# Optimization experiments

Hardware: AMD Instinct MI355X
Metric: run time of the kernel (lower is better)

## Reference

```python
import jax, jax.numpy as jnp
import numpy as np

VOCAB = 128
NUM_PATHS = 100     # num_paths sampled from the lattice
NBEST_SCALE = 0.5   # scale on scores before sampling (k2.random_paths)
TEMPERATURE = 1.0   # logprob temperature before normalization
BLANK = 0           # CTC blank token


def setup_inputs() -> dict:
    key = jax.random.key(0)
    k1, k2, k3, k4 = jax.random.split(key, 4)
    B, T, L = 8, 500, 100
    logits = jax.random.normal(k1, (B, T, VOCAB), jnp.float32)
    emissions = jax.nn.log_softmax(logits, -1)  # acoustic-model log-probs (N, T, C)
    emissions_lengths = jax.random.randint(k2, (B,), 400, T + 1).astype(jnp.int32)
    labels = jax.random.randint(k3, (B, L), 1, VOCAB).astype(jnp.int32)
    labels_length = jax.random.randint(k4, (B,), 80, L + 1).astype(jnp.int32)
    return {"emissions": emissions, "emissions_lengths": emissions_lengths,
            "labels": labels, "labels_length": labels_length}


def _mwer(emissions, emissions_lengths, labels, labels_length):
    B, T, V = emissions.shape
    L = labels.shape[1]
    P = NUM_PATHS
    key = jax.random.key(1)
    # --- N-best path sampling: Gumbel perturbation of nbest_scale-scaled log-probs ---
    u = jax.random.uniform(key, (B, P, T, V), emissions.dtype, 1e-6, 1.0 - 1e-6)
    g = -jnp.log(-jnp.log(u))
    tokens = jnp.argmax(emissions[:, None] * NBEST_SCALE + g, axis=-1)  # (B, P, T)
    frame_mask = jnp.arange(T)[None, None, :] < emissions_lengths[:, None, None]
    # path log-prob under the model (unscaled scores), temperature-scaled
    lp = jnp.take_along_axis(emissions[:, None], tokens[..., None], axis=-1)[..., 0]
    path_logp = jnp.sum(jnp.where(frame_mask, lp, 0.0), axis=-1) / TEMPERATURE  # (B, P)
    # --- CTC collapse (ctc_topo semantics: drop blanks + repeats) into padded hyps ---
    prev = jnp.concatenate([jnp.full_like(tokens[..., :1], -1), tokens[..., :-1]], -1)
    keep = (tokens != BLANK) & (tokens != prev) & frame_mask
    pos = jnp.where(keep, jnp.cumsum(keep, -1) - 1, T)  # dropped frames -> dump slot T
    BP = B * P
    tok2, pos2 = tokens.reshape(BP, T), pos.reshape(BP, T)
    hyp = jnp.full((BP, T + 1), -1, tokens.dtype).at[jnp.arange(BP)[:, None], pos2].set(tok2)[:, :T]
    hyp_len = keep.reshape(BP, T).sum(-1)
    # --- Levenshtein alignment: exact edit distance hyp vs ref (vectorized DP) ---
    refs = jnp.repeat(labels, P, axis=0)             # (BP, L)  hyp_to_ref_map
    ref_len = jnp.repeat(labels_length, P, axis=0)   # (BP,)
    dp0 = jnp.broadcast_to(jnp.arange(L + 1, dtype=jnp.int32), (BP, L + 1))
    js = jnp.arange(L + 1, dtype=jnp.int32)[None, :]

    def step(dp, x):
        h, valid = x  # hyp token (BP,), valid flag (BP,)
        cost = (refs != h[:, None]).astype(jnp.int32)                       # (BP, L)
        cand = jnp.concatenate([dp[:, :1] + 1,
                                jnp.minimum(dp[:, 1:] + 1, dp[:, :-1] + cost)], 1)
        # insertion chain new[j] = min(cand[j], new[j-1]+1) via min-plus prefix
        new = jax.lax.cummin(cand - js, axis=1) + js
        return jnp.where(valid[:, None], new, dp), None

    valid = jnp.arange(T)[:, None] < hyp_len[None, :]  # (T, BP)
    dp, _ = jax.lax.scan(step, dp0, (hyp.T, valid))
    wers = jnp.take_along_axis(dp, ref_len[:, None], 1)[:, 0].reshape(B, P)
    wers = jax.lax.stop_gradient(wers.astype(emissions.dtype))
    # --- MWER: normalize path posteriors per utterance, expected WER, 'mean' ---
    prob = jax.nn.softmax(path_logp, axis=1)
    return jnp.mean(prob * wers)


def reference(emissions, emissions_lengths, labels, labels_length):
    return _mwer(emissions, emissions_lengths, labels, labels_length)
```

## Files before the change

kernel.cpp:

```cpp
#include <hip/hip_runtime.h>
#include <stdint.h>

#define NB 8
#define NP 100
#define NT 500
#define NV 128
#define NBP 800
#define TS 512
#define ES 500
#define PAIRS (NB * NT * 25)

typedef unsigned long long u64;

#define ROTL(x, r) __builtin_amdgcn_alignbit((x), (x), 32 - (r))

__device__ __forceinline__ uint32_t threefry01_lo(uint32_t x0, uint32_t x1) {
  const uint32_t k0 = 0u, k1 = 1u;
  const uint32_t k2 = 0x1BD11BDAu ^ k0 ^ k1;
  x0 += k0; x1 += k1;
#define TF_R(r) { x0 += x1; x1 = ROTL(x1, r); x1 ^= x0; }
  TF_R(13) TF_R(15) TF_R(26) TF_R(6)
  x0 += k1; x1 += k2 + 1u;
  TF_R(17) TF_R(29) TF_R(16) TF_R(24)
  x0 += k2; x1 += k0 + 2u;
  TF_R(13) TF_R(15) TF_R(26) TF_R(6)
  x0 += k0; x1 += k1 + 3u;
  TF_R(17) TF_R(29) TF_R(16) TF_R(24)
  x0 += k1; x1 += k2 + 4u;
  TF_R(13) TF_R(15) TF_R(26) TF_R(6)
  x1 += k0 + 5u;
#undef TF_R
  return x1;
}

__global__ __launch_bounds__(256) void k_sample(
    const float* __restrict__ em, const int* __restrict__ elen,
    uint8_t* __restrict__ tok2, float* __restrict__ lp2t) {
  __shared__ float snw[4][NV + 1];
  const int tid = threadIdx.x;
  const int pi0 = blockIdx.x * 64;
  const int R0 = pi0 / 25;
  for (int i = tid; i < 4 * NV; i += 256) {
    const int r = i >> 7, v = i & 127;
    int R = R0 + r; R = R < NB * NT ? R : NB * NT - 1;
    snw[r][v] = -__builtin_amdgcn_exp2f(em[(size_t)R * NV + v] * -0.7213475204444817f);
  }
  __syncthreads();
  const int gg = blockIdx.x * 256 + tid;
  const int pitem = gg >> 2, q = gg & 3;
  if (pitem >= PAIRS) return;
  const int R = pitem / 25;
  const int pp = pitem - R * 25;
  const int b = R / NT;
  const int t = R - b * NT;
  if (t >= elen[b]) return;
  const int r = R - R0;
  const int vh = q << 5;
  const int bp0 = b * NP + 4 * pp;
  const uint32_t baseA = ((uint32_t)(bp0 * NT + t) << 7) + (uint32_t)vh;
  const uint32_t baseB = baseA + (uint32_t)(NT << 7);
  const uint32_t baseC = baseB + (uint32_t)(NT << 7);
  const uint32_t baseD = baseC + (uint32_t)(NT << 7);
  const float span = (float)(1.0 - 1e-6) - 1e-6f;
  float bvA = 3.0e38f, bvB = 3.0e38f, bvC = 3.0e38f, bvD = 3.0e38f;
  int biA = 0, biB = 0, biC = 0, biD = 0;
#pragma unroll 8
  for (int i = 0; i < 32; i++) {
    const uint32_t rA = threefry01_lo(0u, baseA + (uint32_t)i);
    const uint32_t rB = threefry01_lo(0u, baseB + (uint32_t)i);
    const uint32_t rC = threefry01_lo(0u, baseC + (uint32_t)i);
    const uint32_t rD = threefry01_lo(0u, baseD + (uint32_t)i);
    const float w = snw[r][vh + i];
    const float fA = __uint_as_float((rA >> 9) | 0x3f800000u) - 1.0f;
    const float fB = __uint_as_float((rB >> 9) | 0x3f800000u) - 1.0f;
    const float fC = __uint_as_float((rC >> 9) | 0x3f800000u) - 1.0f;
    const float fD = __uint_as_float((rD >> 9) | 0x3f800000u) - 1.0f;
    const float uA = fmaf(fA, span, 1e-6f);
    const float uB = fmaf(fB, span, 1e-6f);
    const float uC = fmaf(fC, span, 1e-6f);
    const float uD = fmaf(fD, span, 1e-6f);
    const float sA = __log2f(uA) * w;
    const float sB = __log2f(uB) * w;
    const float sC = __log2f(uC) * w;
    const float sD = __log2f(uD) * w;
    if (sA < bvA) { bvA = sA; biA = vh + i; }
    if (sB < bvB) { bvB = sB; biB = vh + i; }
    if (sC < bvC) { bvC = sC; biC = vh + i; }
    if (sD < bvD) { bvD = sD; biD = vh + i; }
  }
#pragma unroll
  for (int off = 1; off <= 2; off <<= 1) {
    float ov; int oi;
    ov = __shfl_xor(bvA, off); oi = __shfl_xor(biA, off);
    if (ov < bvA || (ov == bvA && oi < biA)) { bvA = ov; biA = oi; }
    ov = __shfl_xor(bvB, off); oi = __shfl_xor(biB, off);
    if (ov < bvB || (ov == bvB && oi < biB)) { bvB = ov; biB = oi; }
    ov = __shfl_xor(bvC, off); oi = __shfl_xor(biC, off);
    if (ov < bvC || (ov == bvC && oi < biC)) { bvC = ov; biC = oi; }
    ov = __shfl_xor(bvD, off); oi = __shfl_xor(biD, off);
    if (ov < bvD || (ov == bvD && oi < biD)) { bvD = ov; biD = oi; }
  }
  if (q == 0) {
    const float* __restrict__ erow = em + (size_t)R * NV;
    const float eA = erow[biA], eB = erow[biB], eC = erow[biC], eD = erow[biD];
    tok2[(size_t)(bp0 + 0) * TS + t] = (uint8_t)biA;
    tok2[(size_t)(bp0 + 1) * TS + t] = (uint8_t)biB;
    tok2[(size_t)(bp0 + 2) * TS + t] = (uint8_t)biC;
    tok2[(size_t)(bp0 + 3) * TS + t] = (uint8_t)biD;
    *(float4*)&lp2t[(size_t)t * NBP + bp0] = make_float4(eA, eB, eC, eD);
  }
}

__global__ __launch_bounds__(128) void k_pq(
    const int* __restrict__ labels, const int* __restrict__ llen,
    uint4* __restrict__ pqg) {
  const int b = blockIdx.x;
  const int c = threadIdx.x;
  const int m = llen[b];
  const int* __restrict__ lab = labels + b * 100;
  uint32_t a0 = 0, a1 = 0, a2 = 0, a3 = 0;
  const int e0 = m < 32 ? m : 32, e1 = m < 64 ? m : 64;
  const int e2 = m < 96 ? m : 96, e3 = m;
  for (int i = 0; i < e0; i++)  a0 |= (uint32_t)(lab[i] == c) << i;
  for (int i = 32; i < e1; i++) a1 |= (uint32_t)(lab[i] == c) << (i - 32);
  for (int i = 64; i < e2; i++) a2 |= (uint32_t)(lab[i] == c) << (i - 64);
  for (int i = 96; i < e3; i++) a3 |= (uint32_t)(lab[i] == c) << (i - 96);
  pqg[b * NV + c] = make_uint4(a0, a1, a2, a3);
}

__global__ __launch_bounds__(64) void k_ce(
    const uint8_t* __restrict__ tok2, const uint4* __restrict__ pqg,
    const int* __restrict__ elen, uint4* __restrict__ eqc,
    int* __restrict__ nkept) {
  __shared__ uint4 pqs[NV];
  const int bp = blockIdx.x;
  const int b = bp / NP;
  const int lane = threadIdx.x;
  pqs[lane] = pqg[b * NV + lane];
  pqs[lane + 64] = pqg[b * NV + lane + 64];
  __syncthreads();
  const int el = elen[b];
  const uint8_t* __restrict__ row = tok2 + (size_t)bp * TS;
  uint4* __restrict__ orow = eqc + (size_t)bp * ES;
  int off = 0;
  for (int t0 = 0; t0 < el; t0 += 64) {
    const int t = t0 + lane;
    const bool inb = (t < el);
    const int c = inb ? row[t] : 0;
    const int cp = (t == 0) ? 255 : (inb ? row[t - 1] : 255);
    const bool kept = inb && (c != 0) && (c != cp);
    const u64 mask = __ballot(kept);
    const int idx = off + (int)__builtin_amdgcn_mbcnt_hi(
        (uint32_t)(mask >> 32),
        __builtin_amdgcn_mbcnt_lo((uint32_t)mask, 0u));
    if (kept) orow[idx] = pqs[c];
    off += (int)__popcll(mask);
  }
  if (lane == 0) nkept[bp] = off;
}

__device__ __forceinline__ void loadg(uint4 (&B)[4], int g, const uint4* __restrict__ rowp) {
#pragma unroll
  for (int i = 0; i < 4; i++) {
    int t = g * 4 + i;
    t = t < ES ? t : ES - 1;
    B[i] = rowp[t];
  }
}

__device__ __forceinline__ void procg(const uint4 (&B)[4], int fbase, int nk,
                                      u64 hmask,
                                      u64& Pv0, u64& Pv1, u64& Mv0, u64& Mv1,
                                      int& score, int& scoreFin) {
#pragma unroll
  for (int i = 0; i < 4; i++) {
    const u64 Eq0 = (u64)B[i].x | ((u64)B[i].y << 32);
    const u64 Eq1 = (u64)B[i].z | ((u64)B[i].w << 32);
    const u64 Xv0 = Eq0 | Mv0, Xv1 = Eq1 | Mv1;
    const u64 EP0 = Eq0 & Pv0, EP1 = Eq1 & Pv1;
    const u64 sA = EP0 + Pv0;
    const u64 sB = EP1 + Pv1 + (sA < EP0 ? 1ull : 0ull);
    const u64 Xh0 = (sA ^ Pv0) | Eq0;
    const u64 Xh1 = (sB ^ Pv1) | Eq1;
    const u64 Ph0 = Mv0 | ~(Xh0 | Pv0);
    const u64 Ph1 = Mv1 | ~(Xh1 | Pv1);
    const u64 Mh0 = Pv0 & Xh0, Mh1 = Pv1 & Xh1;
    score += (int)((Ph1 & hmask) != 0) - (int)((Mh1 & hmask) != 0);
    scoreFin = (fbase + i < nk) ? score : scoreFin;
    const u64 nPh1 = (Ph1 << 1) | (Ph0 >> 63);
    const u64 nPh0 = (Ph0 << 1) | 1ull;
    const u64 nMh1 = (Mh1 << 1) | (Mh0 >> 63);
    const u64 nMh0 = (Mh0 << 1);
    Pv0 = nMh0 | ~(Xv0 | nPh0);
    Pv1 = nMh1 | ~(Xv1 | nPh1);
    Mv0 = nPh0 & Xv0;
    Mv1 = nPh1 & Xv1;
  }
}

__global__ __launch_bounds__(64) void k_dp(
    const uint4* __restrict__ eqc, const int* __restrict__ nkept,
    const int* __restrict__ llen, float* __restrict__ wer) {
  const int b = blockIdx.x, h = blockIdx.y;
  const int tid = threadIdx.x;
  const bool active = (tid < 50);
  const int bp = b * NP + h * 50 + (active ? tid : 49);
  const int m = llen[b];
  const int nk = nkept[bp];
  const uint4* __restrict__ rowp = eqc + (size_t)bp * ES;
  u64 Pv0 = ~0ull, Pv1 = ~0ull, Mv0 = 0ull, Mv1 = 0ull;
  int score = m, scoreFin = m;
  const u64 hmask = 1ull << ((m - 1) & 63);

  const int ngl = (nk + 3) >> 2;
  int ngmax = ngl;
  for (int off = 1; off < 64; off <<= 1) {
    const int o = __shfl_xor(ngmax, off);
    ngmax = o > ngmax ? o : ngmax;
  }
  uint4 B0[4], B1[4], B2[4], B3[4];
  loadg(B0, 0, rowp); loadg(B1, 1, rowp);
  loadg(B2, 2, rowp); loadg(B3, 3, rowp);
  int g = 0;
  while (g + 4 <= ngmax) {
    procg(B0, (g    ) * 4, nk, hmask, Pv0, Pv1, Mv0, Mv1, score, scoreFin);
    loadg(B0, g + 4, rowp);
    procg(B1, (g + 1) * 4, nk, hmask, Pv0, Pv1, Mv0, Mv1, score, scoreFin);
    loadg(B1, g + 5, rowp);
    procg(B2, (g + 2) * 4, nk, hmask, Pv0, Pv1, Mv0, Mv1, score, scoreFin);
    loadg(B2, g + 6, rowp);
    procg(B3, (g + 3) * 4, nk, hmask, Pv0, Pv1, Mv0, Mv1, score, scoreFin);
    loadg(B3, g + 7, rowp);
    g += 4;
  }
  if (g     < ngmax) procg(B0, (g    ) * 4, nk, hmask, Pv0, Pv1, Mv0, Mv1, score, scoreFin);
  if (g + 1 < ngmax) procg(B1, (g + 1) * 4, nk, hmask, Pv0, Pv1, Mv0, Mv1, score, scoreFin);
  if (g + 2 < ngmax) procg(B2, (g + 2) * 4, nk, hmask, Pv0, Pv1, Mv0, Mv1, score, scoreFin);
  if (active) wer[bp] = (float)scoreFin;
}

__global__ __launch_bounds__(128) void k_red(
    const float* __restrict__ lp2t, const int* __restrict__ elen,
    double* __restrict__ pred) {
  const int b = blockIdx.x, k = blockIdx.y;
  const int tid = threadIdx.x;
  const bool active = (tid < NP);
  const int p = active ? tid : NP - 1;
  const int el = elen[b];
  const int t0 = k * 125;
  const int t1 = (t0 + 125 < el) ? t0 + 125 : el;
  const float* __restrict__ col = lp2t + b * NP + p;
  double s = 0.0;
#pragma unroll 8
  for (int t = t0; t < t1; t++) s += (double)col[(size_t)t * NBP];
  if (active) pred[(size_t)(b * NP + p) * 4 + k] = s;
}

__global__ __launch_bounds__(512) void k_fin(
    const double* __restrict__ pred, const float* __restrict__ wer,
    float* __restrict__ out) {
  __shared__ float partial[NB];
  const int w = threadIdx.x >> 6, lane = threadIdx.x & 63;
  const int base = w * NP;
  float l0 = -1e30f, l1 = -1e30f;
  if (lane < NP) {
    const double* pr = pred + (size_t)(base + lane) * 4;
    l0 = (float)(pr[0] + pr[1] + pr[2] + pr[3]);
  }
  if (lane + 64 < NP) {
    const double* pr = pred + (size_t)(base + lane + 64) * 4;
    l1 = (float)(pr[0] + pr[1] + pr[2] + pr[3]);
  }
  float mx = fmaxf(l0, l1);
  for (int off = 1; off < 64; off <<= 1) mx = fmaxf(mx, __shfl_xor(mx, off));
  const float e0 = (lane < NP) ? __expf(l0 - mx) : 0.0f;
  const float e1 = (lane + 64 < NP) ? __expf(l1 - mx) : 0.0f;
  const float w0 = (lane < NP) ? wer[base + lane] : 0.0f;
  const float w1 = (lane + 64 < NP) ? wer[base + lane + 64] : 0.0f;
  float s = e0 + e1;
  float a = e0 * w0 + e1 * w1;
  for (int off = 1; off < 64; off <<= 1) {
    s += __shfl_xor(s, off);
    a += __shfl_xor(a, off);
  }
  if (lane == 0) partial[w] = a / s;
  __syncthreads();
  if (threadIdx.x == 0) {
    float tot = 0.0f;
    for (int i = 0; i < NB; i++) tot += partial[i];
    out[0] = tot * (1.0f / (float)NBP);
  }
}

extern "C" void kernel_launch(void* const* d_in, const int* in_sizes, int n_in,
                              void* d_out, int out_size, void* d_ws, size_t ws_size,
                              hipStream_t stream) {
  const float* em     = (const float*)d_in[0];
  const int*   elen   = (const int*)d_in[1];
  const int*   labels = (const int*)d_in[2];
  const int*   llen   = (const int*)d_in[3];
  float* out = (float*)d_out;
  char* ws = (char*)d_ws;
  uint4*   eqc   = (uint4*)ws;
  uint8_t* tok2  = (uint8_t*)(ws + 6400000);
  float*   lp2t  = (float*)(ws + 6809600);
  float*   wer   = (float*)(ws + 8409600);
  double*  pred  = (double*)(ws + 8412800);
  int*     nkept = (int*)(ws + 8438400);
  uint4*   pqg   = (uint4*)(ws + 8441600);

  k_sample<<<dim3((PAIRS * 4 + 255) / 256), dim3(256), 0, stream>>>(em, elen, tok2, lp2t);
  k_pq<<<dim3(NB), dim3(128), 0, stream>>>(labels, llen, pqg);
  k_ce<<<dim3(NBP), dim3(64), 0, stream>>>(tok2, pqg, elen, eqc, nkept);
  k_dp<<<dim3(NB, 2), dim3(64), 0, stream>>>(eqc, nkept, llen, wer);
  k_red<<<dim3(NB, 4), dim3(128), 0, stream>>>(lp2t, elen, pred);
  k_fin<<<dim3(1), dim3(512), 0, stream>>>(pred, wer, out);
}
```

Measured before the change: 228.0 us.

## Merge label-mask and path-logprob reductions into neighboring kernels, pad shared weights

The per-batch label bitmask construction now runs as extra blocks appended to the sampling launch, and the path log-prob column reduction runs as extra blocks alongside the bit-parallel edit-distance kernel. This removes two kernel launches and lets the independent small jobs overlap with larger ones. Shared weights are stored with a padded index to avoid LDS bank conflicts between the four quarter-vocab lanes. The DP step now breaks early past the kept length instead of tracking a masked final score, which adds a data-dependent branch inside the unrolled loop.

```diff
diff --git a/kernel.cpp b/kernel.cpp
--- a/kernel.cpp
+++ b/kernel.cpp
@@ -9,10 +9,13 @@
 #define TS 512
 #define ES 500
 #define PAIRS (NB * NT * 25)
+#define NSB 1563
 
 typedef unsigned long long u64;
 
 #define ROTL(x, r) __builtin_amdgcn_alignbit((x), (x), 32 - (r))
+
+#define SIDX(v) ((v) + ((v) >> 5))
 
 __device__ __forceinline__ uint32_t threefry01_lo(uint32_t x0, uint32_t x1) {
   const uint32_t k0 = 0u, k1 = 1u;
@@ -35,15 +38,34 @@
 
 __global__ __launch_bounds__(256) void k_sample(
     const float* __restrict__ em, const int* __restrict__ elen,
-    uint8_t* __restrict__ tok2, float* __restrict__ lp2t) {
-  __shared__ float snw[4][NV + 1];
+    uint8_t* __restrict__ tok2, float* __restrict__ lp2t,
+    const int* __restrict__ labels, const int* __restrict__ llen,
+    uint4* __restrict__ pqg) {
   const int tid = threadIdx.x;
+  if (blockIdx.x >= NSB) {
+    const int b = blockIdx.x - NSB;
+    if (tid < NV) {
+      const int c = tid;
+      const int m = llen[b];
+      const int* __restrict__ lab = labels + b * 100;
+      uint32_t a0 = 0, a1 = 0, a2 = 0, a3 = 0;
+      const int e0 = m < 32 ? m : 32, e1 = m < 64 ? m : 64;
+      const int e2 = m < 96 ? m : 96, e3 = m;
+      for (int i = 0; i < e0; i++)  a0 |= (uint32_t)(lab[i] == c) << i;
+      for (int i = 32; i < e1; i++) a1 |= (uint32_t)(lab[i] == c) << (i - 32);
+      for (int i = 64; i < e2; i++) a2 |= (uint32_t)(lab[i] == c) << (i - 64);
+      for (int i = 96; i < e3; i++) a3 |= (uint32_t)(lab[i] == c) << (i - 96);
+      pqg[b * NV + c] = make_uint4(a0, a1, a2, a3);
+    }
+    return;
+  }
+  __shared__ float snw[4][NV + 4];
   const int pi0 = blockIdx.x * 64;
   const int R0 = pi0 / 25;
   for (int i = tid; i < 4 * NV; i += 256) {
     const int r = i >> 7, v = i & 127;
     int R = R0 + r; R = R < NB * NT ? R : NB * NT - 1;
-    snw[r][v] = -__builtin_amdgcn_exp2f(em[(size_t)R * NV + v] * -0.7213475204444817f);
+    snw[r][SIDX(v)] = -__builtin_amdgcn_exp2f(em[(size_t)R * NV + v] * -0.7213475204444817f);
   }
   __syncthreads();
   const int gg = blockIdx.x * 256 + tid;
@@ -56,6 +78,7 @@
   if (t >= elen[b]) return;
   const int r = R - R0;
   const int vh = q << 5;
+  const int sbase = vh + q;
   const int bp0 = b * NP + 4 * pp;
   const uint32_t baseA = ((uint32_t)(bp0 * NT + t) << 7) + (uint32_t)vh;
   const uint32_t baseB = baseA + (uint32_t)(NT << 7);
@@ -70,7 +93,7 @@
     const uint32_t rB = threefry01_lo(0u, baseB + (uint32_t)i);
     const uint32_t rC = threefry01_lo(0u, baseC + (uint32_t)i);
     const uint32_t rD = threefry01_lo(0u, baseD + (uint32_t)i);
-    const float w = snw[r][vh + i];
+    const float w = snw[r][sbase + i];
     const float fA = __uint_as_float((rA >> 9) | 0x3f800000u) - 1.0f;
     const float fB = __uint_as_float((rB >> 9) | 0x3f800000u) - 1.0f;
     const float fC = __uint_as_float((rC >> 9) | 0x3f800000u) - 1.0f;
@@ -109,23 +132,6 @@
     tok2[(size_t)(bp0 + 3) * TS + t] = (uint8_t)biD;
     *(float4*)&lp2t[(size_t)t * NBP + bp0] = make_float4(eA, eB, eC, eD);
   }
-}
-
-__global__ __launch_bounds__(128) void k_pq(
-    const int* __restrict__ labels, const int* __restrict__ llen,
-    uint4* __restrict__ pqg) {
-  const int b = blockIdx.x;
-  const int c = threadIdx.x;
-  const int m = llen[b];
-  const int* __restrict__ lab = labels + b * 100;
-  uint32_t a0 = 0, a1 = 0, a2 = 0, a3 = 0;
-  const int e0 = m < 32 ? m : 32, e1 = m < 64 ? m : 64;
-  const int e2 = m < 96 ? m : 96, e3 = m;
-  for (int i = 0; i < e0; i++)  a0 |= (uint32_t)(lab[i] == c) << i;
-  for (int i = 32; i < e1; i++) a1 |= (uint32_t)(lab[i] == c) << (i - 32);
-  for (int i = 64; i < e2; i++) a2 |= (uint32_t)(lab[i] == c) << (i - 64);
-  for (int i = 96; i < e3; i++) a3 |= (uint32_t)(lab[i] == c) << (i - 96);
-  pqg[b * NV + c] = make_uint4(a0, a1, a2, a3);
 }
 
 __global__ __launch_bounds__(64) void k_ce(
@@ -171,9 +177,10 @@
 __device__ __forceinline__ void procg(const uint4 (&B)[4], int fbase, int nk,
                                       u64 hmask,
                                       u64& Pv0, u64& Pv1, u64& Mv0, u64& Mv1,
-                                      int& score, int& scoreFin) {
+                                      int& score) {
 #pragma unroll
   for (int i = 0; i < 4; i++) {
+    if (fbase + i >= nk) break;
     const u64 Eq0 = (u64)B[i].x | ((u64)B[i].y << 32);
     const u64 Eq1 = (u64)B[i].z | ((u64)B[i].w << 32);
     const u64 Xv0 = Eq0 | Mv0, Xv1 = Eq1 | Mv1;
@@ -186,7 +193,6 @@
     const u64 Ph1 = Mv1 | ~(Xh1 | Pv1);
     const u64 Mh0 = Pv0 & Xh0, Mh1 = Pv1 & Xh1;
     score += (int)((Ph1 & hmask) != 0) - (int)((Mh1 & hmask) != 0);
-    scoreFin = (fbase + i < nk) ? score : scoreFin;
     const u64 nPh1 = (Ph1 << 1) | (Ph0 >> 63);
     const u64 nPh0 = (Ph0 << 1) | 1ull;
     const u64 nMh1 = (Mh1 << 1) | (Mh0 >> 63);
@@ -198,18 +204,37 @@
   }
 }
 
-__global__ __launch_bounds__(64) void k_dp(
+__global__ __launch_bounds__(128) void k_dpred(
     const uint4* __restrict__ eqc, const int* __restrict__ nkept,
-    const int* __restrict__ llen, float* __restrict__ wer) {
-  const int b = blockIdx.x, h = blockIdx.y;
+    const int* __restrict__ llen, const float* __restrict__ lp2t,
+    const int* __restrict__ elen, float* __restrict__ wer,
+    double* __restrict__ pred) {
+  const int blk = blockIdx.x;
   const int tid = threadIdx.x;
+  if (blk >= 16) {
+    const int i = blk - 16;
+    const int b = i >> 2, k = i & 3;
+    const bool active = (tid < NP);
+    const int p = active ? tid : NP - 1;
+    const int el = elen[b];
+    const int t0 = k * 125;
+    const int t1 = (t0 + 125 < el) ? t0 + 125 : el;
+    const float* __restrict__ col = lp2t + b * NP + p;
+    double s = 0.0;
+#pragma unroll 8
+    for (int t = t0; t < t1; t++) s += (double)col[(size_t)t * NBP];
+    if (active) pred[(size_t)(b * NP + p) * 4 + k] = s;
+    return;
+  }
+  if (tid >= 64) return;
+  const int b = blk >> 1, h = blk & 1;
   const bool active = (tid < 50);
   const int bp = b * NP + h * 50 + (active ? tid : 49);
   const int m = llen[b];
   const int nk = nkept[bp];
   const uint4* __restrict__ rowp = eqc + (size_t)bp * ES;
   u64 Pv0 = ~0ull, Pv1 = ~0ull, Mv0 = 0ull, Mv1 = 0ull;
-  int score = m, scoreFin = m;
+  int score = m;
   const u64 hmask = 1ull << ((m - 1) & 63);
 
   const int ngl = (nk + 3) >> 2;
@@ -223,37 +248,20 @@
   loadg(B2, 2, rowp); loadg(B3, 3, rowp);
   int g = 0;
   while (g + 4 <= ngmax) {
-    procg(B0, (g    ) * 4, nk, hmask, Pv0, Pv1, Mv0, Mv1, score, scoreFin);
+    procg(B0, (g    ) * 4, nk, hmask, Pv0, Pv1, Mv0, Mv1, score);
     loadg(B0, g + 4, rowp);
-    procg(B1, (g + 1) * 4, nk, hmask, Pv0, Pv1, Mv0, Mv1, score, scoreFin);
+    procg(B1, (g + 1) * 4, nk, hmask, Pv0, Pv1, Mv0, Mv1, score);
     loadg(B1, g + 5, rowp);
-    procg(B2, (g + 2) * 4, nk, hmask, Pv0, Pv1, Mv0, Mv1, score, scoreFin);
+    procg(B2, (g + 2) * 4, nk, hmask, Pv0, Pv1, Mv0, Mv1, score);
     loadg(B2, g + 6, rowp);
-    procg(B3, (g + 3) * 4, nk, hmask, Pv0, Pv1, Mv0, Mv1, score, scoreFin);
+    procg(B3, (g + 3) * 4, nk, hmask, Pv0, Pv1, Mv0, Mv1, score);
     loadg(B3, g + 7, rowp);
     g += 4;
   }
-  if (g     < ngmax) procg(B0, (g    ) * 4, nk, hmask, Pv0, Pv1, Mv0, Mv1, score, scoreFin);
-  if (g + 1 < ngmax) procg(B1, (g + 1) * 4, nk, hmask, Pv0, Pv1, Mv0, Mv1, score, scoreFin);
-  if (g + 2 < ngmax) procg(B2, (g + 2) * 4, nk, hmask, Pv0, Pv1, Mv0, Mv1, score, scoreFin);
-  if (active) wer[bp] = (float)scoreFin;
-}
-
-__global__ __launch_bounds__(128) void k_red(
-    const float* __restrict__ lp2t, const int* __restrict__ elen,
-    double* __restrict__ pred) {
-  const int b = blockIdx.x, k = blockIdx.y;
-  const int tid = threadIdx.x;
-  const bool active = (tid < NP);
-  const int p = active ? tid : NP - 1;
-  const int el = elen[b];
-  const int t0 = k * 125;
-  const int t1 = (t0 + 125 < el) ? t0 + 125 : el;
-  const float* __restrict__ col = lp2t + b * NP + p;
-  double s = 0.0;
-#pragma unroll 8
-  for (int t = t0; t < t1; t++) s += (double)col[(size_t)t * NBP];
-  if (active) pred[(size_t)(b * NP + p) * 4 + k] = s;
+  if (g     < ngmax) procg(B0, (g    ) * 4, nk, hmask, Pv0, Pv1, Mv0, Mv1, score);
+  if (g + 1 < ngmax) procg(B1, (g + 1) * 4, nk, hmask, Pv0, Pv1, Mv0, Mv1, score);
+  if (g + 2 < ngmax) procg(B2, (g + 2) * 4, nk, hmask, Pv0, Pv1, Mv0, Mv1, score);
+  if (active) wer[bp] = (float)score;
 }
 
 __global__ __launch_bounds__(512) void k_fin(
@@ -309,10 +317,9 @@
   int*     nkept = (int*)(ws + 8438400);
   uint4*   pqg   = (uint4*)(ws + 8441600);
 
-  k_sample<<<dim3((PAIRS * 4 + 255) / 256), dim3(256), 0, stream>>>(em, elen, tok2, lp2t);
-  k_pq<<<dim3(NB), dim3(128), 0, stream>>>(labels, llen, pqg);
+  k_sample<<<dim3(NSB + NB), dim3(256), 0, stream>>>(em, elen, tok2, lp2t,
+                                                     labels, llen, pqg);
   k_ce<<<dim3(NBP), dim3(64), 0, stream>>>(tok2, pqg, elen, eqc, nkept);
-  k_dp<<<dim3(NB, 2), dim3(64), 0, stream>>>(eqc, nkept, llen, wer);
-  k_red<<<dim3(NB, 4), dim3(128), 0, stream>>>(lp2t, elen, pred);
+  k_dpred<<<dim3(48), dim3(128), 0, stream>>>(eqc, nkept, llen, lp2t, elen, wer, pred);
   k_fin<<<dim3(1), dim3(512), 0, stream>>>(pred, wer, out);
 }
```

Result: faster. 192.3 us (-15.7%).
